# Optimization experiments

Hardware: AMD Instinct MI355X
Metric: run time of the kernel (lower is better)

## Reference

```python
import jax, jax.numpy as jnp
import numpy as np

D_MODEL, D_STATE, D_INNER = 1024, 16, 2048
B, S = 2, 4096
EPS = 1e-5


def setup_inputs() -> dict:
    key = jax.random.key(0)
    ks = jax.random.split(key, 8)
    return {
        "x": jax.random.normal(ks[0], (B, S, D_MODEL), dtype=jnp.float32),
        "norm_w": jnp.ones((D_MODEL,), jnp.float32),
        "norm_b": jnp.zeros((D_MODEL,), jnp.float32),
        "W_in": jax.random.normal(ks[1], (D_INNER, D_MODEL), jnp.float32) * (1.0 / np.sqrt(D_MODEL)),
        "b_in": jnp.zeros((D_INNER,), jnp.float32),
        "A": jax.random.normal(ks[2], (D_INNER, D_STATE), jnp.float32),
        "B_ssm": jax.random.normal(ks[3], (D_INNER, D_STATE), jnp.float32),
        "C_ssm": jax.random.normal(ks[4], (D_INNER, D_STATE), jnp.float32),
        "W_out": jax.random.normal(ks[5], (D_MODEL, D_INNER), jnp.float32) * (1.0 / np.sqrt(D_INNER)),
        "b_out": jnp.zeros((D_MODEL,), jnp.float32),
    }


def reference(x, norm_w, norm_b, W_in, b_in, A, B_ssm, C_ssm, W_out, b_out):
    residual = x
    # LayerNorm
    mu = jnp.mean(x, axis=-1, keepdims=True)
    var = jnp.mean(jnp.square(x - mu), axis=-1, keepdims=True)
    xn = (x - mu) * jax.lax.rsqrt(var + EPS) * norm_w + norm_b
    # in_proj -> [B, S, d_inner]
    h = jnp.einsum("bsd,ed->bse", xn, W_in) + b_in
    # per-step gates / inputs over d_state
    a = jax.nn.sigmoid(jnp.einsum("bse,en->bsn", h, A))  # decay gate [B,S,n]
    u = jnp.einsum("bse,en->bsn", h, B_ssm)              # input drive [B,S,n]
    # diagonal SSM recurrence: s_t = s_{t-1} * a_t + u_t
    def step(s, inp):
        a_t, u_t = inp
        s = s * a_t + u_t
        return s, s
    s0 = jnp.zeros((x.shape[0], D_STATE), x.dtype)
    _, states = jax.lax.scan(step, s0, (jnp.swapaxes(a, 0, 1), jnp.swapaxes(u, 0, 1)))
    # states: [S, B, n] -> readout y_t = s_t @ C^T : [B, S, d_inner]
    y = jnp.einsum("sbn,en->bse", states, C_ssm)
    out = jnp.einsum("bse,de->bsd", y, W_out) + b_out
    return out + residual
```

## Files before the change

kernel.cpp:

```cpp
#include <hip/hip_runtime.h>
#include <cstddef>
#include <cstdint>

#define D_MODEL 1024
#define D_STATE 16
#define D_INNER 2048
#define BATCH 2
#define SEQ 4096
#define NTOK (BATCH * SEQ)
#define EPS_LN 1e-5f

#define WS_PA 0
#define WS_PB 16384
#define WS_M 32768
#define WS_CA 49152
#define WS_CB 49168
#define WS_TP 49184
#define WS_UP 49312
#define WS_A 49440
#define WS_U (WS_A + NTOK * 16)
#define WS_S (WS_U + NTOK * 16)
#define WS_PPA (WS_S + NTOK * 16)
#define WS_PPB (WS_PPA + 64 * 16384)
#define WS_PM (WS_PPB + 64 * 16384)

__global__ __launch_bounds__(256) void pa_pb_kernel(
    const float* __restrict__ W_in, const float* __restrict__ A,
    const float* __restrict__ Bs, float* __restrict__ ws) {
  __shared__ float4 lds4[3 * 16 * 32];
  const int bid = blockIdx.x;
  const int tid = threadIdx.x;
  const int lane = tid & 63;
  const int wv = tid >> 6;
  const int mat = bid >> 9;
  const int bb = bid & 511;
  const int dg = bb >> 6;
  const int ec = bb & 63;
  const int dl = tid & 31;
  const int eo = tid >> 5;

  const float4* __restrict__ W4 = reinterpret_cast<const float4*>(W_in);
  const float4* __restrict__ P4 =
      reinterpret_cast<const float4*>(mat == 0 ? A : Bs);

  float4 acc[16];
#pragma unroll
  for (int n = 0; n < 16; ++n) acc[n] = make_float4(0.f, 0.f, 0.f, 0.f);

#pragma unroll
  for (int k = 0; k < 4; ++k) {
    const int e = ec * 32 + eo * 4 + k;
    const float4 w4 = W4[(size_t)e * 256 + dg * 32 + dl];
    float4 pe[4];
#pragma unroll
    for (int q = 0; q < 4; ++q) pe[q] = P4[(size_t)e * 4 + q];
#pragma unroll
    for (int q = 0; q < 4; ++q) {
      const float p0 = pe[q].x, p1 = pe[q].y, p2 = pe[q].z, p3 = pe[q].w;
      acc[q * 4 + 0].x = fmaf(w4.x, p0, acc[q * 4 + 0].x);
      acc[q * 4 + 0].y = fmaf(w4.y, p0, acc[q * 4 + 0].y);
      acc[q * 4 + 0].z = fmaf(w4.z, p0, acc[q * 4 + 0].z);
      acc[q * 4 + 0].w = fmaf(w4.w, p0, acc[q * 4 + 0].w);
      acc[q * 4 + 1].x = fmaf(w4.x, p1, acc[q * 4 + 1].x);
      acc[q * 4 + 1].y = fmaf(w4.y, p1, acc[q * 4 + 1].y);
      acc[q * 4 + 1].z = fmaf(w4.z, p1, acc[q * 4 + 1].z);
      acc[q * 4 + 1].w = fmaf(w4.w, p1, acc[q * 4 + 1].w);
      acc[q * 4 + 2].x = fmaf(w4.x, p2, acc[q * 4 + 2].x);
      acc[q * 4 + 2].y = fmaf(w4.y, p2, acc[q * 4 + 2].y);
      acc[q * 4 + 2].z = fmaf(w4.z, p2, acc[q * 4 + 2].z);
      acc[q * 4 + 2].w = fmaf(w4.w, p2, acc[q * 4 + 2].w);
      acc[q * 4 + 3].x = fmaf(w4.x, p3, acc[q * 4 + 3].x);
      acc[q * 4 + 3].y = fmaf(w4.y, p3, acc[q * 4 + 3].y);
      acc[q * 4 + 3].z = fmaf(w4.z, p3, acc[q * 4 + 3].z);
      acc[q * 4 + 3].w = fmaf(w4.w, p3, acc[q * 4 + 3].w);
    }
  }
#pragma unroll
  for (int n = 0; n < 16; ++n) {
    acc[n].x += __shfl_xor(acc[n].x, 32);
    acc[n].y += __shfl_xor(acc[n].y, 32);
    acc[n].z += __shfl_xor(acc[n].z, 32);
    acc[n].w += __shfl_xor(acc[n].w, 32);
  }
  if (wv >= 1 && lane < 32) {
#pragma unroll
    for (int n = 0; n < 16; ++n) lds4[(wv - 1) * 512 + n * 32 + lane] = acc[n];
  }
  __syncthreads();
  if (wv == 0 && lane < 32) {
    float* pp = ws + (mat == 0 ? WS_PPA : WS_PPB);
    float4* pp4 = reinterpret_cast<float4*>(pp);
#pragma unroll
    for (int n = 0; n < 16; ++n) {
      const float4 a0 = lds4[n * 32 + lane];
      const float4 a1 = lds4[512 + n * 32 + lane];
      const float4 a2 = lds4[1024 + n * 32 + lane];
      float4 r = acc[n];
      r.x += a0.x + a1.x + a2.x;
      r.y += a0.y + a1.y + a2.y;
      r.z += a0.z + a1.z + a2.z;
      r.w += a0.w + a1.w + a2.w;
      pp4[(size_t)(ec * 16 + n) * 256 + dg * 32 + lane] = r;
    }
  }
}

__global__ __launch_bounds__(256) void mt_kernel(
    const float* __restrict__ W_out, const float* __restrict__ C,
    const float* __restrict__ A, const float* __restrict__ Bs,
    const float* __restrict__ b_in, float* __restrict__ ws) {
  __shared__ float ct[16 * 132];
  const int bid = blockIdx.x;
  const int tid = threadIdx.x;
  const int lane = tid & 63;
  const int wv = tid >> 6;

  if (bid < 2048) {
    const int dg = bid >> 4;
    const int ec = bid & 15;
    const int td = tid >> 5;
    const int te = tid & 31;
    const int e0 = ec * 128;
    const float4* __restrict__ W4 = reinterpret_cast<const float4*>(W_out);
    const float4* __restrict__ C4 = reinterpret_cast<const float4*>(C);
#pragma unroll
    for (int r = 0; r < 2; ++r) {
      const int idx = r * 256 + tid;
      const int el = idx >> 2;
      const int q = idx & 3;
      const float4 cv = C4[(size_t)(e0 + el) * 4 + q];
      ct[(q * 4 + 0) * 132 + el] = cv.x;
      ct[(q * 4 + 1) * 132 + el] = cv.y;
      ct[(q * 4 + 2) * 132 + el] = cv.z;
      ct[(q * 4 + 3) * 132 + el] = cv.w;
    }
    __syncthreads();
    const int d = dg * 8 + td;
    const float4 w4 = W4[(size_t)d * 512 + ec * 32 + te];
    const float4* __restrict__ ct4 = reinterpret_cast<const float4*>(ct);
    float acc[16];
#pragma unroll
    for (int n = 0; n < 16; ++n) {
      const float4 cv = ct4[n * 33 + te];
      acc[n] = w4.x * cv.x + w4.y * cv.y + w4.z * cv.z + w4.w * cv.w;
    }
#pragma unroll
    for (int off = 1; off < 32; off <<= 1) {
#pragma unroll
      for (int n = 0; n < 16; ++n) acc[n] += __shfl_xor(acc[n], off);
    }
    if (te == 0) {
      float* pm = ws + WS_PM;
#pragma unroll
      for (int n = 0; n < 16; ++n)
        pm[(size_t)(ec * 16 + n) * 1024 + d] = acc[n];
    }
  } else {
    const int which = bid - 2048;
    const float* __restrict__ P = (which == 0) ? A : Bs;
    __shared__ float red[64];
    float acc[16];
#pragma unroll
    for (int n = 0; n < 16; ++n) acc[n] = 0.f;
    for (int e = tid; e < D_INNER; e += 256) {
      const float w = b_in[e];
      const float* pe = P + (size_t)e * 16;
#pragma unroll
      for (int n = 0; n < 16; ++n) acc[n] = fmaf(w, pe[n], acc[n]);
    }
#pragma unroll
    for (int n = 0; n < 16; ++n) {
#pragma unroll
      for (int off = 32; off; off >>= 1) acc[n] += __shfl_xor(acc[n], off);
    }
    if (lane == 0) {
#pragma unroll
      for (int n = 0; n < 16; ++n) red[wv * 16 + n] = acc[n];
    }
    __syncthreads();
    if (tid < 16) {
      ws[WS_CA + which * 16 + tid] =
          red[tid] + red[16 + tid] + red[32 + tid] + red[48 + tid];
    }
  }
}

__global__ __launch_bounds__(256) void reduce_kernel(
    const float* __restrict__ nw, const float* __restrict__ nb,
    float* __restrict__ ws) {
  __shared__ float4 red4[256];
  const int bid = blockIdx.x;
  const int tid = threadIdx.x;
  const int grp = bid >> 6;
  const int sub = bid & 63;
  const int n = sub >> 2;
  const int dq = sub & 3;
  const int dl = tid & 63;
  const int cg = tid >> 6;
  const float4* __restrict__ pp4 = reinterpret_cast<const float4*>(
      ws + (grp == 0 ? WS_PPA : (grp == 1 ? WS_PPB : WS_PM)));
  const int base = n * 256 + dq * 64 + dl;

  float4 acc = make_float4(0.f, 0.f, 0.f, 0.f);
  if (grp < 2) {
#pragma unroll
    for (int j = 0; j < 16; ++j) {
      const float4 v = pp4[(size_t)(cg * 16 + j) * 4096 + base];
      acc.x += v.x;
      acc.y += v.y;
      acc.z += v.z;
      acc.w += v.w;
    }
  } else {
#pragma unroll
    for (int j = 0; j < 4; ++j) {
      const float4 v = pp4[(size_t)(cg * 4 + j) * 4096 + base];
      acc.x += v.x;
      acc.y += v.y;
      acc.z += v.z;
      acc.w += v.w;
    }
  }
  red4[cg * 64 + dl] = acc;
  __syncthreads();
  if (tid < 64) {
    const float4 a1 = red4[64 + dl];
    const float4 a2 = red4[128 + dl];
    const float4 a3 = red4[192 + dl];
    float4 r = red4[dl];
    r.x += a1.x + a2.x + a3.x;
    r.y += a1.y + a2.y + a3.y;
    r.z += a1.z + a2.z + a3.z;
    r.w += a1.w + a2.w + a3.w;
    if (grp == 2) {
      reinterpret_cast<float4*>(ws + WS_M)[n * 256 + dq * 64 + dl] = r;
    } else {
      const float4 w4 = reinterpret_cast<const float4*>(nw)[dq * 64 + dl];
      const float4 b4 = reinterpret_cast<const float4*>(nb)[dq * 64 + dl];
      float4 vf;
      vf.x = r.x * w4.x;
      vf.y = r.y * w4.y;
      vf.z = r.z * w4.z;
      vf.w = r.w * w4.w;
      reinterpret_cast<float4*>(ws + (grp == 0 ? WS_PA : WS_PB))
          [n * 256 + dq * 64 + dl] = vf;
      float tP = vf.x + vf.y + vf.z + vf.w;
      float uP = b4.x * r.x + b4.y * r.y + b4.z * r.z + b4.w * r.w;
#pragma unroll
      for (int off = 32; off; off >>= 1) {
        tP += __shfl_xor(tP, off);
        uP += __shfl_xor(uP, off);
      }
      if (dl == 0) {
        ws[WS_TP + grp * 64 + n * 4 + dq] = tP;
        ws[WS_UP + grp * 64 + n * 4 + dq] = uP;
      }
    }
  }
}

__global__ __launch_bounds__(256) void token_kernel(
    const float* __restrict__ x, const float* __restrict__ ws,
    float* __restrict__ a_t, float* __restrict__ u_t) {
  __shared__ float4 lds4[32 * 69];
  const int tid = threadIdx.x;
  const int lane = tid & 63;
  const int wv = tid >> 6;
  const int g = lane >> 4;
  const int np = lane & 15;
  const int t0 = blockIdx.x * 32 + wv * 8;

  const float4* __restrict__ x4 = reinterpret_cast<const float4*>(x);
  const float4* __restrict__ ws4 = reinterpret_cast<const float4*>(ws);

  float sum[8], sq[8], SA[8], SB[8];
#pragma unroll
  for (int t = 0; t < 8; ++t) {
    sum[t] = 0.f;
    sq[t] = 0.f;
    SA[t] = 0.f;
    SB[t] = 0.f;
  }

  for (int p = 0; p < 4; ++p) {
    __syncthreads();
#pragma unroll
    for (int i = 0; i < 8; ++i) {
      const int idx = i * 256 + tid;
      const int r = idx >> 6;
      const int u = idx & 63;
      lds4[r * 69 + u + (u >> 4)] = ws4[(size_t)r * 256 + p * 64 + u];
    }
    __syncthreads();
#pragma unroll
    for (int t = 0; t < 8; ++t) {
      const float4 xs = x4[(size_t)(t0 + t) * 256 + p * 64 + lane];
      sum[t] += xs.x + xs.y + xs.z + xs.w;
      sq[t] = fmaf(xs.x, xs.x, sq[t]);
      sq[t] = fmaf(xs.y, xs.y, sq[t]);
      sq[t] = fmaf(xs.z, xs.z, sq[t]);
      sq[t] = fmaf(xs.w, xs.w, sq[t]);
    }
#pragma unroll
    for (int j = 0; j < 16; ++j) {
      const float4 pa = lds4[np * 69 + g * 17 + j];
      const float4 pb = lds4[(16 + np) * 69 + g * 17 + j];
#pragma unroll
      for (int t = 0; t < 8; ++t) {
        const float4 xb = x4[(size_t)(t0 + t) * 256 + p * 64 + g * 16 + j];
        SA[t] = fmaf(xb.x, pa.x, SA[t]);
        SA[t] = fmaf(xb.y, pa.y, SA[t]);
        SA[t] = fmaf(xb.z, pa.z, SA[t]);
        SA[t] = fmaf(xb.w, pa.w, SA[t]);
        SB[t] = fmaf(xb.x, pb.x, SB[t]);
        SB[t] = fmaf(xb.y, pb.y, SB[t]);
        SB[t] = fmaf(xb.z, pb.z, SB[t]);
        SB[t] = fmaf(xb.w, pb.w, SB[t]);
      }
    }
  }
#pragma unroll
  for (int t = 0; t < 8; ++t) {
    float s = sum[t], q = sq[t];
#pragma unroll
    for (int off = 32; off; off >>= 1) {
      s += __shfl_xor(s, off);
      q += __shfl_xor(q, off);
    }
    const float mu = s * (1.0f / 1024.0f);
    const float var = fmaf(-mu, mu, q * (1.0f / 1024.0f));
    const float rstd = rsqrtf(var + EPS_LN);
    float sa = SA[t] + __shfl_xor(SA[t], 16);
    sa += __shfl_xor(sa, 32);
    float sb = SB[t] + __shfl_xor(SB[t], 16);
    sb += __shfl_xor(sb, 32);
    if (g == 0) {
      const float* tp = ws + WS_TP;
      const float* up = ws + WS_UP;
      const float TA = tp[np * 4] + tp[np * 4 + 1] + tp[np * 4 + 2] +
                       tp[np * 4 + 3];
      const float TB = tp[64 + np * 4] + tp[64 + np * 4 + 1] +
                       tp[64 + np * 4 + 2] + tp[64 + np * 4 + 3];
      const float cA = ws[WS_CA + np] + up[np * 4] + up[np * 4 + 1] +
                       up[np * 4 + 2] + up[np * 4 + 3];
      const float cB = ws[WS_CB + np] + up[64 + np * 4] + up[64 + np * 4 + 1] +
                       up[64 + np * 4 + 2] + up[64 + np * 4 + 3];
      const float zA = fmaf(rstd, fmaf(-mu, TA, sa), cA);
      const float zB = fmaf(rstd, fmaf(-mu, TB, sb), cB);
      const int tok = t0 + t;
      const int bb = tok >> 12;
      const int ss = tok & 4095;
      const size_t row = (size_t)(bb * 16 + np) * 4096 + ss;
      a_t[row] = 1.0f / (1.0f + __expf(-zA));
      u_t[row] = zB;
    }
  }
}

__global__ __launch_bounds__(256) void scan_kernel(
    const float* __restrict__ a_t, const float* __restrict__ u_t,
    float* __restrict__ st_t) {
  const int seq = blockIdx.x;
  const int tid = threadIdx.x;
  const int lane = tid & 63;
  const int wv = tid >> 6;
  const size_t rowbase = (size_t)seq * 4096;
  const float4* __restrict__ a4 =
      reinterpret_cast<const float4*>(a_t + rowbase) + tid * 4;
  const float4* __restrict__ u4 =
      reinterpret_cast<const float4*>(u_t + rowbase) + tid * 4;

  float4 av[4], uv[4];
#pragma unroll
  for (int q = 0; q < 4; ++q) {
    av[q] = a4[q];
    uv[q] = u4[q];
  }
  float Ag = 1.f, Ug = 0.f;
#pragma unroll
  for (int q = 0; q < 4; ++q) {
    Ug = fmaf(Ug, av[q].x, uv[q].x);
    Ag *= av[q].x;
    Ug = fmaf(Ug, av[q].y, uv[q].y);
    Ag *= av[q].y;
    Ug = fmaf(Ug, av[q].z, uv[q].z);
    Ag *= av[q].z;
    Ug = fmaf(Ug, av[q].w, uv[q].w);
    Ag *= av[q].w;
  }
#pragma unroll
  for (int off = 1; off < 64; off <<= 1) {
    const float Ap = __shfl_up(Ag, off);
    const float Up = __shfl_up(Ug, off);
    if (lane >= off) {
      Ug = fmaf(Up, Ag, Ug);
      Ag = Ap * Ag;
    }
  }
  __shared__ float sA[4], sU[4];
  if (lane == 63) {
    sA[wv] = Ag;
    sU[wv] = Ug;
  }
  __syncthreads();
  float c = 0.f;
  for (int w = 0; w < wv; ++w) c = fmaf(c, sA[w], sU[w]);
  const float Ae = __shfl_up(Ag, 1);
  const float Ue = __shfl_up(Ug, 1);
  const float carry = (lane == 0) ? c : fmaf(c, Ae, Ue);
  float s = carry;
  float4* __restrict__ st4 =
      reinterpret_cast<float4*>(st_t + rowbase) + tid * 4;
#pragma unroll
  for (int q = 0; q < 4; ++q) {
    float4 ov;
    s = fmaf(s, av[q].x, uv[q].x);
    ov.x = s;
    s = fmaf(s, av[q].y, uv[q].y);
    ov.y = s;
    s = fmaf(s, av[q].z, uv[q].z);
    ov.z = s;
    s = fmaf(s, av[q].w, uv[q].w);
    ov.w = s;
    st4[q] = ov;
  }
}

__global__ __launch_bounds__(256) void out_kernel(
    const float* __restrict__ x, const float* __restrict__ ws,
    const float* __restrict__ b_out, float* __restrict__ out) {
  const int tid = threadIdx.x;
  const int lane = tid & 63;
  const int wv = tid >> 6;
  const int t0 = blockIdx.x * 16 + wv * 4;
  const int bb = t0 >> 12;
  const int s0 = t0 & 4095;
  const float4* __restrict__ x4 = reinterpret_cast<const float4*>(x);
  const float4* __restrict__ M4 = reinterpret_cast<const float4*>(ws + WS_M);
  const float4* __restrict__ b4 = reinterpret_cast<const float4*>(b_out);
  const float* __restrict__ st = ws + WS_S;
  float4* __restrict__ o4 = reinterpret_cast<float4*>(out);

  float s[4][16];
#pragma unroll
  for (int n = 0; n < 16; ++n) {
    const float* row = st + (size_t)(bb * 16 + n) * 4096 + s0;
#pragma unroll
    for (int tt = 0; tt < 4; ++tt) s[tt][n] = row[tt];
  }

#pragma unroll
  for (int k = 0; k < 4; ++k) {
    const float4 bv = b4[k * 64 + lane];
    float4 acc[4];
#pragma unroll
    for (int tt = 0; tt < 4; ++tt) {
      const float4 xv = x4[(size_t)(t0 + tt) * 256 + k * 64 + lane];
      acc[tt] =
          make_float4(xv.x + bv.x, xv.y + bv.y, xv.z + bv.z, xv.w + bv.w);
    }
#pragma unroll
    for (int n = 0; n < 16; ++n) {
      const float4 m = M4[(size_t)n * 256 + k * 64 + lane];
#pragma unroll
      for (int tt = 0; tt < 4; ++tt) {
        acc[tt].x = fmaf(s[tt][n], m.x, acc[tt].x);
        acc[tt].y = fmaf(s[tt][n], m.y, acc[tt].y);
        acc[tt].z = fmaf(s[tt][n], m.z, acc[tt].z);
        acc[tt].w = fmaf(s[tt][n], m.w, acc[tt].w);
      }
    }
#pragma unroll
    for (int tt = 0; tt < 4; ++tt)
      o4[(size_t)(t0 + tt) * 256 + k * 64 + lane] = acc[tt];
  }
}

extern "C" void kernel_launch(void* const* d_in, const int* in_sizes, int n_in,
                              void* d_out, int out_size, void* d_ws,
                              size_t ws_size, hipStream_t stream) {
  const float* x = (const float*)d_in[0];
  const float* norm_w = (const float*)d_in[1];
  const float* norm_b = (const float*)d_in[2];
  const float* W_in = (const float*)d_in[3];
  const float* b_in = (const float*)d_in[4];
  const float* A = (const float*)d_in[5];
  const float* B_ssm = (const float*)d_in[6];
  const float* C_ssm = (const float*)d_in[7];
  const float* W_out = (const float*)d_in[8];
  const float* b_out = (const float*)d_in[9];
  float* ws = (float*)d_ws;
  float* out = (float*)d_out;

  pa_pb_kernel<<<1024, 256, 0, stream>>>(W_in, A, B_ssm, ws);
  mt_kernel<<<2050, 256, 0, stream>>>(W_out, C_ssm, A, B_ssm, b_in, ws);
  reduce_kernel<<<192, 256, 0, stream>>>(norm_w, norm_b, ws);
  token_kernel<<<256, 256, 0, stream>>>(x, ws, ws + WS_A, ws + WS_U);
  scan_kernel<<<32, 256, 0, stream>>>(ws + WS_A, ws + WS_U, ws + WS_S);
  out_kernel<<<512, 256, 0, stream>>>(x, ws, b_out, out);
}
```

Measured before the change: 78.67 us.

## Merge weight-precompute kernels and halve tokens per block in token/out kernels

Combines the two independent weight-precompute kernels into a single launch with block-index dispatch, removing one launch and letting both parts fill the GPU together. Halves the tokens each wave handles in token_kernel and out_kernel and doubles their grids, giving more blocks across the compute units. Hoists the per-state constant loads out of the token loop. The trade-off is less reuse of the loaded projection and matrix data per block, and a larger shared-memory footprint in the merged kernel.

New measurement: 70.85 us. 9.9% less time.

```diff
diff --git a/kernel.cpp b/kernel.cpp
--- a/kernel.cpp
+++ b/kernel.cpp
@@ -24,100 +24,96 @@
 #define WS_PPB (WS_PPA + 64 * 16384)
 #define WS_PM (WS_PPB + 64 * 16384)
 
-__global__ __launch_bounds__(256) void pa_pb_kernel(
-    const float* __restrict__ W_in, const float* __restrict__ A,
-    const float* __restrict__ Bs, float* __restrict__ ws) {
-  __shared__ float4 lds4[3 * 16 * 32];
+__global__ __launch_bounds__(256) void weights_kernel(
+    const float* __restrict__ W_in, const float* __restrict__ W_out,
+    const float* __restrict__ C, const float* __restrict__ A,
+    const float* __restrict__ Bs, const float* __restrict__ b_in,
+    float* __restrict__ ws) {
+  __shared__ float4 smem4[1536];
   const int bid = blockIdx.x;
   const int tid = threadIdx.x;
   const int lane = tid & 63;
   const int wv = tid >> 6;
-  const int mat = bid >> 9;
-  const int bb = bid & 511;
-  const int dg = bb >> 6;
-  const int ec = bb & 63;
-  const int dl = tid & 31;
-  const int eo = tid >> 5;
-
-  const float4* __restrict__ W4 = reinterpret_cast<const float4*>(W_in);
-  const float4* __restrict__ P4 =
-      reinterpret_cast<const float4*>(mat == 0 ? A : Bs);
-
-  float4 acc[16];
-#pragma unroll
-  for (int n = 0; n < 16; ++n) acc[n] = make_float4(0.f, 0.f, 0.f, 0.f);
-
-#pragma unroll
-  for (int k = 0; k < 4; ++k) {
-    const int e = ec * 32 + eo * 4 + k;
-    const float4 w4 = W4[(size_t)e * 256 + dg * 32 + dl];
-    float4 pe[4];
-#pragma unroll
-    for (int q = 0; q < 4; ++q) pe[q] = P4[(size_t)e * 4 + q];
-#pragma unroll
-    for (int q = 0; q < 4; ++q) {
-      const float p0 = pe[q].x, p1 = pe[q].y, p2 = pe[q].z, p3 = pe[q].w;
-      acc[q * 4 + 0].x = fmaf(w4.x, p0, acc[q * 4 + 0].x);
-      acc[q * 4 + 0].y = fmaf(w4.y, p0, acc[q * 4 + 0].y);
-      acc[q * 4 + 0].z = fmaf(w4.z, p0, acc[q * 4 + 0].z);
-      acc[q * 4 + 0].w = fmaf(w4.w, p0, acc[q * 4 + 0].w);
-      acc[q * 4 + 1].x = fmaf(w4.x, p1, acc[q * 4 + 1].x);
-      acc[q * 4 + 1].y = fmaf(w4.y, p1, acc[q * 4 + 1].y);
-      acc[q * 4 + 1].z = fmaf(w4.z, p1, acc[q * 4 + 1].z);
-      acc[q * 4 + 1].w = fmaf(w4.w, p1, acc[q * 4 + 1].w);
-      acc[q * 4 + 2].x = fmaf(w4.x, p2, acc[q * 4 + 2].x);
-      acc[q * 4 + 2].y = fmaf(w4.y, p2, acc[q * 4 + 2].y);
-      acc[q * 4 + 2].z = fmaf(w4.z, p2, acc[q * 4 + 2].z);
-      acc[q * 4 + 2].w = fmaf(w4.w, p2, acc[q * 4 + 2].w);
-      acc[q * 4 + 3].x = fmaf(w4.x, p3, acc[q * 4 + 3].x);
-      acc[q * 4 + 3].y = fmaf(w4.y, p3, acc[q * 4 + 3].y);
-      acc[q * 4 + 3].z = fmaf(w4.z, p3, acc[q * 4 + 3].z);
-      acc[q * 4 + 3].w = fmaf(w4.w, p3, acc[q * 4 + 3].w);
-    }
-  }
-#pragma unroll
-  for (int n = 0; n < 16; ++n) {
-    acc[n].x += __shfl_xor(acc[n].x, 32);
-    acc[n].y += __shfl_xor(acc[n].y, 32);
-    acc[n].z += __shfl_xor(acc[n].z, 32);
-    acc[n].w += __shfl_xor(acc[n].w, 32);
-  }
-  if (wv >= 1 && lane < 32) {
-#pragma unroll
-    for (int n = 0; n < 16; ++n) lds4[(wv - 1) * 512 + n * 32 + lane] = acc[n];
-  }
-  __syncthreads();
-  if (wv == 0 && lane < 32) {
-    float* pp = ws + (mat == 0 ? WS_PPA : WS_PPB);
-    float4* pp4 = reinterpret_cast<float4*>(pp);
+
+  if (bid < 1024) {
+    float4* lds4 = smem4;
+    const int mat = bid >> 9;
+    const int bb = bid & 511;
+    const int dg = bb >> 6;
+    const int ec = bb & 63;
+    const int dl = tid & 31;
+    const int eo = tid >> 5;
+
+    const float4* __restrict__ W4 = reinterpret_cast<const float4*>(W_in);
+    const float4* __restrict__ P4 =
+        reinterpret_cast<const float4*>(mat == 0 ? A : Bs);
+
+    float4 acc[16];
+#pragma unroll
+    for (int n = 0; n < 16; ++n) acc[n] = make_float4(0.f, 0.f, 0.f, 0.f);
+
+#pragma unroll
+    for (int k = 0; k < 4; ++k) {
+      const int e = ec * 32 + eo * 4 + k;
+      const float4 w4 = W4[(size_t)e * 256 + dg * 32 + dl];
+      float4 pe[4];
+#pragma unroll
+      for (int q = 0; q < 4; ++q) pe[q] = P4[(size_t)e * 4 + q];
+#pragma unroll
+      for (int q = 0; q < 4; ++q) {
+        const float p0 = pe[q].x, p1 = pe[q].y, p2 = pe[q].z, p3 = pe[q].w;
+        acc[q * 4 + 0].x = fmaf(w4.x, p0, acc[q * 4 + 0].x);
+        acc[q * 4 + 0].y = fmaf(w4.y, p0, acc[q * 4 + 0].y);
+        acc[q * 4 + 0].z = fmaf(w4.z, p0, acc[q * 4 + 0].z);
+        acc[q * 4 + 0].w = fmaf(w4.w, p0, acc[q * 4 + 0].w);
+        acc[q * 4 + 1].x = fmaf(w4.x, p1, acc[q * 4 + 1].x);
+        acc[q * 4 + 1].y = fmaf(w4.y, p1, acc[q * 4 + 1].y);
+        acc[q * 4 + 1].z = fmaf(w4.z, p1, acc[q * 4 + 1].z);
+        acc[q * 4 + 1].w = fmaf(w4.w, p1, acc[q * 4 + 1].w);
+        acc[q * 4 + 2].x = fmaf(w4.x, p2, acc[q * 4 + 2].x);
+        acc[q * 4 + 2].y = fmaf(w4.y, p2, acc[q * 4 + 2].y);
+        acc[q * 4 + 2].z = fmaf(w4.z, p2, acc[q * 4 + 2].z);
+        acc[q * 4 + 2].w = fmaf(w4.w, p2, acc[q * 4 + 2].w);
+        acc[q * 4 + 3].x = fmaf(w4.x, p3, acc[q * 4 + 3].x);
+        acc[q * 4 + 3].y = fmaf(w4.y, p3, acc[q * 4 + 3].y);
+        acc[q * 4 + 3].z = fmaf(w4.z, p3, acc[q * 4 + 3].z);
+        acc[q * 4 + 3].w = fmaf(w4.w, p3, acc[q * 4 + 3].w);
+      }
+    }
 #pragma unroll
     for (int n = 0; n < 16; ++n) {
-      const float4 a0 = lds4[n * 32 + lane];
-      const float4 a1 = lds4[512 + n * 32 + lane];
-      const float4 a2 = lds4[1024 + n * 32 + lane];
-      float4 r = acc[n];
-      r.x += a0.x + a1.x + a2.x;
-      r.y += a0.y + a1.y + a2.y;
-      r.z += a0.z + a1.z + a2.z;
-      r.w += a0.w + a1.w + a2.w;
-      pp4[(size_t)(ec * 16 + n) * 256 + dg * 32 + lane] = r;
-    }
-  }
-}
-
-__global__ __launch_bounds__(256) void mt_kernel(
-    const float* __restrict__ W_out, const float* __restrict__ C,
-    const float* __restrict__ A, const float* __restrict__ Bs,
-    const float* __restrict__ b_in, float* __restrict__ ws) {
-  __shared__ float ct[16 * 132];
-  const int bid = blockIdx.x;
-  const int tid = threadIdx.x;
-  const int lane = tid & 63;
-  const int wv = tid >> 6;
-
-  if (bid < 2048) {
-    const int dg = bid >> 4;
-    const int ec = bid & 15;
+      acc[n].x += __shfl_xor(acc[n].x, 32);
+      acc[n].y += __shfl_xor(acc[n].y, 32);
+      acc[n].z += __shfl_xor(acc[n].z, 32);
+      acc[n].w += __shfl_xor(acc[n].w, 32);
+    }
+    if (wv >= 1 && lane < 32) {
+#pragma unroll
+      for (int n = 0; n < 16; ++n)
+        lds4[(wv - 1) * 512 + n * 32 + lane] = acc[n];
+    }
+    __syncthreads();
+    if (wv == 0 && lane < 32) {
+      float* pp = ws + (mat == 0 ? WS_PPA : WS_PPB);
+      float4* pp4 = reinterpret_cast<float4*>(pp);
+#pragma unroll
+      for (int n = 0; n < 16; ++n) {
+        const float4 a0 = lds4[n * 32 + lane];
+        const float4 a1 = lds4[512 + n * 32 + lane];
+        const float4 a2 = lds4[1024 + n * 32 + lane];
+        float4 r = acc[n];
+        r.x += a0.x + a1.x + a2.x;
+        r.y += a0.y + a1.y + a2.y;
+        r.z += a0.z + a1.z + a2.z;
+        r.w += a0.w + a1.w + a2.w;
+        pp4[(size_t)(ec * 16 + n) * 256 + dg * 32 + lane] = r;
+      }
+    }
+  } else if (bid < 3072) {
+    float* ct = reinterpret_cast<float*>(smem4);
+    const int mb = bid - 1024;
+    const int dg = mb >> 4;
+    const int ec = mb & 15;
     const int td = tid >> 5;
     const int te = tid & 31;
     const int e0 = ec * 128;
@@ -156,9 +152,9 @@
         pm[(size_t)(ec * 16 + n) * 1024 + d] = acc[n];
     }
   } else {
-    const int which = bid - 2048;
+    float* red = reinterpret_cast<float*>(smem4);
+    const int which = bid - 3072;
     const float* __restrict__ P = (which == 0) ? A : Bs;
-    __shared__ float red[64];
     float acc[16];
 #pragma unroll
     for (int n = 0; n < 16; ++n) acc[n] = 0.f;
@@ -268,14 +264,25 @@
   const int wv = tid >> 6;
   const int g = lane >> 4;
   const int np = lane & 15;
-  const int t0 = blockIdx.x * 32 + wv * 8;
+  const int t0 = blockIdx.x * 16 + wv * 4;
 
   const float4* __restrict__ x4 = reinterpret_cast<const float4*>(x);
   const float4* __restrict__ ws4 = reinterpret_cast<const float4*>(ws);
 
-  float sum[8], sq[8], SA[8], SB[8];
-#pragma unroll
-  for (int t = 0; t < 8; ++t) {
+  const float* tp = ws + WS_TP;
+  const float* up = ws + WS_UP;
+  const float TA =
+      tp[np * 4] + tp[np * 4 + 1] + tp[np * 4 + 2] + tp[np * 4 + 3];
+  const float TB = tp[64 + np * 4] + tp[64 + np * 4 + 1] +
+                   tp[64 + np * 4 + 2] + tp[64 + np * 4 + 3];
+  const float cA = ws[WS_CA + np] + up[np * 4] + up[np * 4 + 1] +
+                   up[np * 4 + 2] + up[np * 4 + 3];
+  const float cB = ws[WS_CB + np] + up[64 + np * 4] + up[64 + np * 4 + 1] +
+                   up[64 + np * 4 + 2] + up[64 + np * 4 + 3];
+
+  float sum[4], sq[4], SA[4], SB[4];
+#pragma unroll
+  for (int t = 0; t < 4; ++t) {
     sum[t] = 0.f;
     sq[t] = 0.f;
     SA[t] = 0.f;
@@ -293,7 +300,7 @@
     }
     __syncthreads();
 #pragma unroll
-    for (int t = 0; t < 8; ++t) {
+    for (int t = 0; t < 4; ++t) {
       const float4 xs = x4[(size_t)(t0 + t) * 256 + p * 64 + lane];
       sum[t] += xs.x + xs.y + xs.z + xs.w;
       sq[t] = fmaf(xs.x, xs.x, sq[t]);
@@ -306,7 +313,7 @@
       const float4 pa = lds4[np * 69 + g * 17 + j];
       const float4 pb = lds4[(16 + np) * 69 + g * 17 + j];
 #pragma unroll
-      for (int t = 0; t < 8; ++t) {
+      for (int t = 0; t < 4; ++t) {
         const float4 xb = x4[(size_t)(t0 + t) * 256 + p * 64 + g * 16 + j];
         SA[t] = fmaf(xb.x, pa.x, SA[t]);
         SA[t] = fmaf(xb.y, pa.y, SA[t]);
@@ -320,7 +327,7 @@
     }
   }
 #pragma unroll
-  for (int t = 0; t < 8; ++t) {
+  for (int t = 0; t < 4; ++t) {
     float s = sum[t], q = sq[t];
 #pragma unroll
     for (int off = 32; off; off >>= 1) {
@@ -335,16 +342,6 @@
     float sb = SB[t] + __shfl_xor(SB[t], 16);
     sb += __shfl_xor(sb, 32);
     if (g == 0) {
-      const float* tp = ws + WS_TP;
-      const float* up = ws + WS_UP;
-      const float TA = tp[np * 4] + tp[np * 4 + 1] + tp[np * 4 + 2] +
-                       tp[np * 4 + 3];
-      const float TB = tp[64 + np * 4] + tp[64 + np * 4 + 1] +
-                       tp[64 + np * 4 + 2] + tp[64 + np * 4 + 3];
-      const float cA = ws[WS_CA + np] + up[np * 4] + up[np * 4 + 1] +
-                       up[np * 4 + 2] + up[np * 4 + 3];
-      const float cB = ws[WS_CB + np] + up[64 + np * 4] + up[64 + np * 4 + 1] +
-                       up[64 + np * 4 + 2] + up[64 + np * 4 + 3];
       const float zA = fmaf(rstd, fmaf(-mu, TA, sa), cA);
       const float zB = fmaf(rstd, fmaf(-mu, TB, sb), cB);
       const int tok = t0 + t;
@@ -432,7 +429,7 @@
   const int tid = threadIdx.x;
   const int lane = tid & 63;
   const int wv = tid >> 6;
-  const int t0 = blockIdx.x * 16 + wv * 4;
+  const int t0 = blockIdx.x * 8 + wv * 2;
   const int bb = t0 >> 12;
   const int s0 = t0 & 4095;
   const float4* __restrict__ x4 = reinterpret_cast<const float4*>(x);
@@ -441,20 +438,20 @@
   const float* __restrict__ st = ws + WS_S;
   float4* __restrict__ o4 = reinterpret_cast<float4*>(out);
 
-  float s[4][16];
+  float s[2][16];
 #pragma unroll
   for (int n = 0; n < 16; ++n) {
     const float* row = st + (size_t)(bb * 16 + n) * 4096 + s0;
 #pragma unroll
-    for (int tt = 0; tt < 4; ++tt) s[tt][n] = row[tt];
+    for (int tt = 0; tt < 2; ++tt) s[tt][n] = row[tt];
   }
 
 #pragma unroll
   for (int k = 0; k < 4; ++k) {
     const float4 bv = b4[k * 64 + lane];
-    float4 acc[4];
-#pragma unroll
-    for (int tt = 0; tt < 4; ++tt) {
+    float4 acc[2];
+#pragma unroll
+    for (int tt = 0; tt < 2; ++tt) {
       const float4 xv = x4[(size_t)(t0 + tt) * 256 + k * 64 + lane];
       acc[tt] =
           make_float4(xv.x + bv.x, xv.y + bv.y, xv.z + bv.z, xv.w + bv.w);
@@ -463,7 +460,7 @@
     for (int n = 0; n < 16; ++n) {
       const float4 m = M4[(size_t)n * 256 + k * 64 + lane];
 #pragma unroll
-      for (int tt = 0; tt < 4; ++tt) {
+      for (int tt = 0; tt < 2; ++tt) {
         acc[tt].x = fmaf(s[tt][n], m.x, acc[tt].x);
         acc[tt].y = fmaf(s[tt][n], m.y, acc[tt].y);
         acc[tt].z = fmaf(s[tt][n], m.z, acc[tt].z);
@@ -471,7 +468,7 @@
       }
     }
 #pragma unroll
-    for (int tt = 0; tt < 4; ++tt)
+    for (int tt = 0; tt < 2; ++tt)
       o4[(size_t)(t0 + tt) * 256 + k * 64 + lane] = acc[tt];
   }
 }
@@ -492,10 +489,10 @@
   float* ws = (float*)d_ws;
   float* out = (float*)d_out;
 
-  pa_pb_kernel<<<1024, 256, 0, stream>>>(W_in, A, B_ssm, ws);
-  mt_kernel<<<2050, 256, 0, stream>>>(W_out, C_ssm, A, B_ssm, b_in, ws);
+  weights_kernel<<<3074, 256, 0, stream>>>(W_in, W_out, C_ssm, A, B_ssm, b_in,
+                                           ws);
   reduce_kernel<<<192, 256, 0, stream>>>(norm_w, norm_b, ws);
-  token_kernel<<<256, 256, 0, stream>>>(x, ws, ws + WS_A, ws + WS_U);
+  token_kernel<<<512, 256, 0, stream>>>(x, ws, ws + WS_A, ws + WS_U);
   scan_kernel<<<32, 256, 0, stream>>>(ws + WS_A, ws + WS_U, ws + WS_S);
-  out_kernel<<<512, 256, 0, stream>>>(x, ws, b_out, out);
-}
+  out_kernel<<<1024, 256, 0, stream>>>(x, ws, b_out, out);
+}
```
